# Optimization experiments

Hardware: AMD Instinct MI355X
Metric: run time of the kernel (lower is better)

Reference implementation:

```python
import jax, jax.numpy as jnp
import numpy as np

N_U = 8192
N_C = 8192
D_IN = 32
D_HID = 32  # hidden_dim == output_dim (required by the concat->Linear shape)


def _glorot(key, fan_in, fan_out):
    r = np.sqrt(6.0 / (fan_in + fan_out)).astype(np.float32)
    return jax.random.uniform(key, (fan_in, fan_out), jnp.float32, -r, r)


def setup_inputs() -> dict:
    key = jax.random.key(0)
    ks = jax.random.split(key, 12)
    X_U = jax.random.normal(ks[0], (N_U, D_IN), jnp.float32)
    X_C = jax.random.normal(ks[1], (N_C, D_IN), jnp.float32)
    adj_uu = jax.random.uniform(ks[2], (N_U, N_U), jnp.float32)
    adj_uc = jax.random.uniform(ks[3], (N_U, N_C), jnp.float32)
    adj_cc = jax.random.uniform(ks[4], (N_C, N_C), jnp.float32)
    weight_s = _glorot(ks[5], D_IN, D_HID)          # GCN_S.weight (shared for uu and cc)
    proj_u = _glorot(ks[6], D_IN, D_HID)            # GCN_C.projection_u
    proj_c = _glorot(ks[7], D_IN, D_HID)            # GCN_C.projection_c (unused in fwd math)
    weight_c = _glorot(ks[8], D_HID, D_HID)         # GCN_C.weight
    W_lin = jax.random.normal(ks[9], (D_IN + D_HID, D_HID), jnp.float32) * 0.05  # Linear, no bias
    a_vec = jax.random.normal(ks[10], (D_HID, 1), jnp.float32) * 0.05            # attention vector
    return {"X_U": X_U, "X_C": X_C, "adj_uu": adj_uu, "adj_uc": adj_uc, "adj_cc": adj_cc,
            "weight_s": weight_s, "proj_u": proj_u, "proj_c": proj_c,
            "weight_c": weight_c, "W_lin": W_lin, "a_vec": a_vec}


def gcn_s(adj, x, w):
    # D^-1/2 A D^-1/2 (X W), with D = 1 + rowsum(A); expressed as broadcast scaling
    dinv = jax.lax.rsqrt(1.0 + jnp.sum(adj, axis=1))  # [N]
    support = x @ w                                    # [N, d]
    return dinv[:, None] * (adj @ (dinv[:, None] * support))


def gcn_c(adj, x_u, p_u, w):
    # Du^-1/2 A Dc^-1/2 ((X_U P_u) W); projected_c is computed but unused upstream
    du = jax.lax.rsqrt(jnp.sum(adj, axis=1))  # [N_u]
    dc = jax.lax.rsqrt(jnp.sum(adj, axis=0))  # [N_c]
    support = (x_u @ p_u) @ w                  # [N_u, d]
    return du[:, None] * (adj @ (dc[:, None] * support))  # wait: see note below


def gcn_c_correct(adj, x_u, p_u, w):
    # norm_adj = diag(du) @ adj @ diag(dc)  -> [N_u, N_c]; output = norm_adj @ support ([N_u,d])
    # Actually original multiplies [N_u,N_c] norm_adj by support built from X_U [N_u,d]:
    # this only typechecks when N_u == N_c (as in the repo's usage). We keep that math.
    du = jax.lax.rsqrt(jnp.sum(adj, axis=1))
    dc = jax.lax.rsqrt(jnp.sum(adj, axis=0))
    support = (x_u @ p_u) @ w
    return du[:, None] * (adj @ (dc[:, None] * support))


def reference(X_U, X_C, adj_uu, adj_uc, adj_cc, weight_s, proj_u, proj_c, weight_c, W_lin, a_vec):
    node_embed_u = gcn_s(adj_uu, X_U, weight_s)            # [N_u, d]
    node_embed_c1 = gcn_s(adj_cc, X_C, weight_s)           # [N_c, d]
    node_embed_c2 = gcn_c_correct(adj_uc, X_U, proj_u, weight_c)  # [N_c, d]

    a_tau_1 = jax.nn.relu(jnp.concatenate([node_embed_c1, X_C], axis=-1) @ W_lin) @ a_vec  # [N_c,1]
    a_tau_2 = jax.nn.relu(jnp.concatenate([node_embed_c2, X_C], axis=-1) @ W_lin) @ a_vec  # [N_c,1]
    e_tau = jax.nn.softmax(jnp.concatenate([a_tau_1, a_tau_2], axis=1), axis=1)            # [N_c,2]

    Y_c = e_tau[:, 0:1] * node_embed_c1
    Y_u = e_tau[:, 1:2] * node_embed_c2
    node_embed_c = Y_c + Y_u
    return (node_embed_u, node_embed_c, Y_c, Y_u)
```

## Files before the change

kernel.cpp:

```cpp
#include <hip/hip_runtime.h>
#include <hip/hip_bf16.h>

#define N_NODES 8192

typedef __attribute__((ext_vector_type(8))) short short8;
typedef __attribute__((ext_vector_type(8))) unsigned short ushort8;
typedef __attribute__((ext_vector_type(4))) unsigned short ushort4v;
typedef __attribute__((ext_vector_type(4))) float floatx4;

__device__ inline unsigned short f2bf(float f) {
  unsigned int u = __float_as_uint(f);
  u = (u + 0x7FFFu + ((u >> 16) & 1u)) >> 16;
  return (unsigned short)u;
}

__device__ inline float waveSum(float s) {
#pragma unroll
  for (int off = 32; off >= 1; off >>= 1) s += __shfl_xor(s, off, 64);
  return s;
}

__device__ inline void acc4(float4& a, const float4 b) {
  a.x += b.x; a.y += b.y; a.z += b.z; a.w += b.w;
}
__device__ inline float hsum4(const float4 v) { return v.x + v.y + v.z + v.w; }

__global__ __launch_bounds__(256) void k_rowsum(const float* __restrict__ a_uu,
                                                const float* __restrict__ a_cc,
                                                float* __restrict__ dinv_uu,
                                                float* __restrict__ dinv_cc) {
  const float* A = (blockIdx.y == 0) ? a_uu : a_cc;
  float* dv = (blockIdx.y == 0) ? dinv_uu : dinv_cc;
  int w = threadIdx.x >> 6, l = threadIdx.x & 63;
  long row = (long)blockIdx.x * 4 + w;
  const float* rp = A + row * N_NODES + 4 * l;
  float s = 0.f;
#pragma unroll 2
  for (int i = 0; i < 32; i += 4) {
    float4 v0 = *(const float4*)(rp + 256 * (i + 0));
    float4 v1 = *(const float4*)(rp + 256 * (i + 1));
    float4 v2 = *(const float4*)(rp + 256 * (i + 2));
    float4 v3 = *(const float4*)(rp + 256 * (i + 3));
    s += hsum4(v0) + hsum4(v1) + hsum4(v2) + hsum4(v3);
  }
  s = waveSum(s);
  if (l == 0) dv[row] = rsqrtf(1.0f + s);
}

__global__ __launch_bounds__(256) void k_uc_partials(const float* __restrict__ adj,
                                                     float* __restrict__ rs_part,
                                                     float* __restrict__ cs_part) {
  __shared__ float cacc[4][1024];
  int t = threadIdx.x, w = t >> 6, l = t & 63;
  int rc = blockIdx.x, cc = blockIdx.y;
  int c0 = cc * 1024;
  int rbase = rc * 128 + w * 32;
  float4 ca0 = {0, 0, 0, 0}, ca1 = {0, 0, 0, 0}, ca2 = {0, 0, 0, 0}, ca3 = {0, 0, 0, 0};
  for (int kr = 0; kr < 32; kr += 2) {
    const float* p0 = adj + (long)(rbase + kr) * N_NODES + c0 + 4 * l;
    const float* p1 = p0 + N_NODES;
    float4 u0 = *(const float4*)(p0 + 0);
    float4 u1 = *(const float4*)(p0 + 256);
    float4 u2 = *(const float4*)(p0 + 512);
    float4 u3 = *(const float4*)(p0 + 768);
    float4 v0 = *(const float4*)(p1 + 0);
    float4 v1 = *(const float4*)(p1 + 256);
    float4 v2 = *(const float4*)(p1 + 512);
    float4 v3 = *(const float4*)(p1 + 768);
    acc4(ca0, u0); acc4(ca1, u1); acc4(ca2, u2); acc4(ca3, u3);
    acc4(ca0, v0); acc4(ca1, v1); acc4(ca2, v2); acc4(ca3, v3);
    float s0 = hsum4(u0) + hsum4(u1) + hsum4(u2) + hsum4(u3);
    float s1 = hsum4(v0) + hsum4(v1) + hsum4(v2) + hsum4(v3);
    s0 = waveSum(s0);
    s1 = waveSum(s1);
    if (l == 0) {
      rs_part[(long)cc * N_NODES + rbase + kr] = s0;
      rs_part[(long)cc * N_NODES + rbase + kr + 1] = s1;
    }
  }
  *(float4*)&cacc[w][0 + 4 * l] = ca0;
  *(float4*)&cacc[w][256 + 4 * l] = ca1;
  *(float4*)&cacc[w][512 + 4 * l] = ca2;
  *(float4*)&cacc[w][768 + 4 * l] = ca3;
  __syncthreads();
#pragma unroll
  for (int i = 0; i < 4; ++i) {
    int c = t + 256 * i;
    cs_part[(long)rc * N_NODES + c0 + c] = cacc[0][c] + cacc[1][c] + cacc[2][c] + cacc[3][c];
  }
}

__global__ __launch_bounds__(256) void k_finalize(const float* __restrict__ rs_part,
                                                  const float* __restrict__ cs_part,
                                                  float* __restrict__ du,
                                                  float* __restrict__ dc) {
  int i = blockIdx.x * 256 + threadIdx.x;
  float s = 0.f;
#pragma unroll
  for (int cc = 0; cc < 8; ++cc) s += rs_part[(long)cc * N_NODES + i];
  du[i] = rsqrtf(s);
  float c = 0.f;
#pragma unroll
  for (int rc = 0; rc < 64; ++rc) c += cs_part[(long)rc * N_NODES + i];
  dc[i] = rsqrtf(c);
}

__global__ void k_projw(const float* __restrict__ proj_u,
                        const float* __restrict__ weight_c, float* __restrict__ P) {
  int t = threadIdx.x;
  int i = t >> 5, j = t & 31;
  float s = 0.f;
#pragma unroll
  for (int k = 0; k < 32; ++k) s += proj_u[i * 32 + k] * weight_c[k * 32 + j];
  P[t] = s;
}

__global__ __launch_bounds__(256) void k_support(
    const float* __restrict__ X_U, const float* __restrict__ X_C,
    const float* __restrict__ weight_s, const float* __restrict__ P,
    const float* __restrict__ dinv_uu, const float* __restrict__ dinv_cc,
    const float* __restrict__ dc,
    unsigned short* __restrict__ bt_uu, unsigned short* __restrict__ bt_cc,
    unsigned short* __restrict__ bt_uc) {
  int m = blockIdx.y;
  const float* X = (m == 1) ? X_C : X_U;
  const float* W = (m == 2) ? P : weight_s;
  const float* dv = (m == 0) ? dinv_uu : (m == 1) ? dinv_cc : dc;
  unsigned short* bt = (m == 0) ? bt_uu : (m == 1) ? bt_cc : bt_uc;
  __shared__ float Wl[32][32];
  __shared__ float Xl[8][32];
  int t = threadIdx.x;
#pragma unroll
  for (int i = 0; i < 4; ++i) {
    int idx = t + 256 * i;
    Wl[idx >> 5][idx & 31] = W[idx];
  }
  int r = t >> 5, n = t & 31;
  int j0 = blockIdx.x * 8;
  Xl[r][n] = X[(long)(j0 + r) * 32 + n];
  __syncthreads();
  float s = 0.f;
#pragma unroll
  for (int k = 0; k < 32; ++k) s += Xl[r][k] * Wl[k][n];
  s *= dv[j0 + r];
  bt[(long)n * N_NODES + j0 + r] = f2bf(s);
}

__global__ __launch_bounds__(256) void k_gemm(
    const float* __restrict__ adj_uu, const float* __restrict__ adj_cc,
    const float* __restrict__ adj_uc,
    const unsigned short* __restrict__ bt_uu, const unsigned short* __restrict__ bt_cc,
    const unsigned short* __restrict__ bt_uc,
    const float* __restrict__ dinv_uu, const float* __restrict__ dinv_cc,
    const float* __restrict__ du,
    float* __restrict__ out_u, float* __restrict__ c1, float* __restrict__ c2) {
  int m = blockIdx.y;
  const float* adj = (m == 0) ? adj_uu : (m == 1) ? adj_cc : adj_uc;
  const unsigned short* bt = (m == 0) ? bt_uu : (m == 1) ? bt_cc : bt_uc;
  const float* dsc = (m == 0) ? dinv_uu : (m == 1) ? dinv_cc : du;
  float* outp = (m == 0) ? out_u : (m == 1) ? c1 : c2;

  __shared__ unsigned short As[32][136];
  __shared__ unsigned short Bs[32][136];

  int t = threadIdx.x;
  int w = t >> 6, l = t & 63;
  int mh = w & 1, nh = w >> 1;
  long r0 = (long)blockIdx.x * 32;

  int ar = t >> 3, ac = (t & 7) * 4;
  int bn = t >> 3, bk = (t & 7) * 8;

  const float* ap = adj + (r0 + ar) * N_NODES + ac;
  const unsigned short* bp = bt + (long)bn * N_NODES + bk;

  float4 a0 = *(const float4*)(ap + 0);
  float4 a1 = *(const float4*)(ap + 32);
  float4 a2 = *(const float4*)(ap + 64);
  float4 a3 = *(const float4*)(ap + 96);
  ushort8 b0 = *(const ushort8*)(bp + 0);
  ushort8 b1 = *(const ushort8*)(bp + 64);

  floatx4 acc = {0.f, 0.f, 0.f, 0.f};

  for (int step = 0; step < 64; ++step) {
    ushort4v q;
    q.x = f2bf(a0.x); q.y = f2bf(a0.y); q.z = f2bf(a0.z); q.w = f2bf(a0.w);
    *(ushort4v*)&As[ar][ac + 0] = q;
    q.x = f2bf(a1.x); q.y = f2bf(a1.y); q.z = f2bf(a1.z); q.w = f2bf(a1.w);
    *(ushort4v*)&As[ar][ac + 32] = q;
    q.x = f2bf(a2.x); q.y = f2bf(a2.y); q.z = f2bf(a2.z); q.w = f2bf(a2.w);
    *(ushort4v*)&As[ar][ac + 64] = q;
    q.x = f2bf(a3.x); q.y = f2bf(a3.y); q.z = f2bf(a3.z); q.w = f2bf(a3.w);
    *(ushort4v*)&As[ar][ac + 96] = q;
    *(ushort8*)&Bs[bn][bk + 0] = b0;
    *(ushort8*)&Bs[bn][bk + 64] = b1;
    __syncthreads();

    if (step < 63) {
      ap += 128; bp += 128;
      a0 = *(const float4*)(ap + 0);
      a1 = *(const float4*)(ap + 32);
      a2 = *(const float4*)(ap + 64);
      a3 = *(const float4*)(ap + 96);
      b0 = *(const ushort8*)(bp + 0);
      b1 = *(const ushort8*)(bp + 64);
    }

#pragma unroll
    for (int kk = 0; kk < 4; ++kk) {
      short8 af = *(const short8*)&As[16 * mh + (l & 15)][kk * 32 + (l >> 4) * 8];
      short8 bf = *(const short8*)&Bs[16 * nh + (l & 15)][kk * 32 + (l >> 4) * 8];
      acc = __builtin_amdgcn_mfma_f32_16x16x32_bf16(af, bf, acc, 0, 0, 0);
    }
    __syncthreads();
  }

  int mrow = (int)r0 + 16 * mh + ((l >> 4) << 2);
  int ncol = 16 * nh + (l & 15);
#pragma unroll
  for (int r = 0; r < 4; ++r) {
    float sc = dsc[mrow + r];
    outp[(long)(mrow + r) * 32 + ncol] = sc * acc[r];
  }
}

__global__ __launch_bounds__(256) void k_epilogue(
    const float* __restrict__ c1, const float* __restrict__ c2,
    const float* __restrict__ X_C, const float* __restrict__ W_lin,
    const float* __restrict__ a_vec, float* __restrict__ out) {
  __shared__ float Wl[64][32];
  __shared__ float al[32];
  int t = threadIdx.x;
#pragma unroll
  for (int i = 0; i < 8; ++i) {
    int idx = t + 256 * i;
    Wl[idx >> 5][idx & 31] = W_lin[idx];
  }
  if (t < 32) al[t] = a_vec[t];
  int g = t >> 5, n = t & 31;
  long row = (long)blockIdx.x * 8 + g;
  __syncthreads();
  float h1 = c1[row * 32 + n];
  float h2 = c2[row * 32 + n];
  float xv = X_C[row * 32 + n];
  float s1 = 0.f, s2 = 0.f, sx = 0.f;
#pragma unroll
  for (int k = 0; k < 32; ++k) {
    float h1k = __shfl(h1, k, 32);
    float h2k = __shfl(h2, k, 32);
    float xk = __shfl(xv, k, 32);
    float w0 = Wl[k][n], w1 = Wl[32 + k][n];
    s1 += h1k * w0;
    s2 += h2k * w0;
    sx += xk * w1;
  }
  float t1 = fmaxf(s1 + sx, 0.f) * al[n];
  float t2 = fmaxf(s2 + sx, 0.f) * al[n];
#pragma unroll
  for (int off = 16; off >= 1; off >>= 1) {
    t1 += __shfl_xor(t1, off, 32);
    t2 += __shfl_xor(t2, off, 32);
  }
  float mx = fmaxf(t1, t2);
  float e1 = expf(t1 - mx), e2 = expf(t2 - mx);
  float inv = 1.0f / (e1 + e2);
  float w1w = e1 * inv, w2w = e2 * inv;
  float yc = w1w * h1, yu = w2w * h2;
  long o = row * 32 + n;
  out[262144 + o] = yc + yu;
  out[524288 + o] = yc;
  out[786432 + o] = yu;
}

extern "C" void kernel_launch(void* const* d_in, const int* in_sizes, int n_in,
                              void* d_out, int out_size, void* d_ws, size_t ws_size,
                              hipStream_t stream) {
  (void)in_sizes; (void)n_in; (void)out_size; (void)ws_size;
  const float* X_U = (const float*)d_in[0];
  const float* X_C = (const float*)d_in[1];
  const float* adj_uu = (const float*)d_in[2];
  const float* adj_uc = (const float*)d_in[3];
  const float* adj_cc = (const float*)d_in[4];
  const float* weight_s = (const float*)d_in[5];
  const float* proj_u = (const float*)d_in[6];
  const float* weight_c = (const float*)d_in[8];
  const float* W_lin = (const float*)d_in[9];
  const float* a_vec = (const float*)d_in[10];
  float* out = (float*)d_out;

  char* ws = (char*)d_ws;
  auto alloc = [&](size_t bytes) {
    char* p = ws;
    ws += (bytes + 255) & ~(size_t)255;
    return p;
  };
  float* dinv_uu = (float*)alloc(8192 * 4);
  float* dinv_cc = (float*)alloc(8192 * 4);
  float* du = (float*)alloc(8192 * 4);
  float* dc = (float*)alloc(8192 * 4);
  float* rs_part = (float*)alloc((size_t)8 * 8192 * 4);
  float* cs_part = (float*)alloc((size_t)64 * 8192 * 4);
  float* P = (float*)alloc(1024 * 4);
  float* c1 = (float*)alloc((size_t)262144 * 4);
  float* c2 = (float*)alloc((size_t)262144 * 4);
  unsigned short* bt_uu = (unsigned short*)alloc((size_t)262144 * 2);
  unsigned short* bt_cc = (unsigned short*)alloc((size_t)262144 * 2);
  unsigned short* bt_uc = (unsigned short*)alloc((size_t)262144 * 2);

  hipLaunchKernelGGL(k_rowsum, dim3(2048, 2), dim3(256), 0, stream,
                     adj_uu, adj_cc, dinv_uu, dinv_cc);
  hipLaunchKernelGGL(k_uc_partials, dim3(64, 8), dim3(256), 0, stream,
                     adj_uc, rs_part, cs_part);
  hipLaunchKernelGGL(k_finalize, dim3(32), dim3(256), 0, stream,
                     rs_part, cs_part, du, dc);
  hipLaunchKernelGGL(k_projw, dim3(1), dim3(1024), 0, stream, proj_u, weight_c, P);
  hipLaunchKernelGGL(k_support, dim3(1024, 3), dim3(256), 0, stream,
                     X_U, X_C, weight_s, P, dinv_uu, dinv_cc, dc, bt_uu, bt_cc, bt_uc);
  hipLaunchKernelGGL(k_gemm, dim3(256, 3), dim3(256), 0, stream,
                     adj_uu, adj_cc, adj_uc, bt_uu, bt_cc, bt_uc,
                     dinv_uu, dinv_cc, du, out, c1, c2);
  hipLaunchKernelGGL(k_epilogue, dim3(1024), dim3(256), 0, stream,
                     c1, c2, X_C, W_lin, a_vec, out);
}
```

Measured before the change: 847.5 us.

## Replace LDS-tiled GEMM with single-wave register MFMA kernel and split-K partials

After: 877.8 us. 3.6% more time.

```diff
diff --git a/kernel.cpp b/kernel.cpp
--- a/kernel.cpp
+++ b/kernel.cpp
@@ -4,8 +4,6 @@
 #define N_NODES 8192
 
 typedef __attribute__((ext_vector_type(8))) short short8;
-typedef __attribute__((ext_vector_type(8))) unsigned short ushort8;
-typedef __attribute__((ext_vector_type(4))) unsigned short ushort4v;
 typedef __attribute__((ext_vector_type(4))) float floatx4;
 
 __device__ inline unsigned short f2bf(float f) {
@@ -14,6 +12,15 @@
   return (unsigned short)u;
 }
 
+__device__ inline short8 cvt8(const float4 lo, const float4 hi) {
+  short8 r;
+  r[0] = (short)f2bf(lo.x); r[1] = (short)f2bf(lo.y);
+  r[2] = (short)f2bf(lo.z); r[3] = (short)f2bf(lo.w);
+  r[4] = (short)f2bf(hi.x); r[5] = (short)f2bf(hi.y);
+  r[6] = (short)f2bf(hi.z); r[7] = (short)f2bf(hi.w);
+  return r;
+}
+
 __device__ inline float waveSum(float s) {
 #pragma unroll
   for (int off = 32; off >= 1; off >>= 1) s += __shfl_xor(s, off, 64);
@@ -25,12 +32,8 @@
 }
 __device__ inline float hsum4(const float4 v) { return v.x + v.y + v.z + v.w; }
 
-__global__ __launch_bounds__(256) void k_rowsum(const float* __restrict__ a_uu,
-                                                const float* __restrict__ a_cc,
-                                                float* __restrict__ dinv_uu,
-                                                float* __restrict__ dinv_cc) {
-  const float* A = (blockIdx.y == 0) ? a_uu : a_cc;
-  float* dv = (blockIdx.y == 0) ? dinv_uu : dinv_cc;
+__global__ __launch_bounds__(256) void k_rowsum(const float* __restrict__ A,
+                                                float* __restrict__ dv) {
   int w = threadIdx.x >> 6, l = threadIdx.x & 63;
   long row = (long)blockIdx.x * 4 + w;
   const float* rp = A + row * N_NODES + 4 * l;
@@ -115,18 +118,10 @@
   P[t] = s;
 }
 
-__global__ __launch_bounds__(256) void k_support(
-    const float* __restrict__ X_U, const float* __restrict__ X_C,
-    const float* __restrict__ weight_s, const float* __restrict__ P,
-    const float* __restrict__ dinv_uu, const float* __restrict__ dinv_cc,
-    const float* __restrict__ dc,
-    unsigned short* __restrict__ bt_uu, unsigned short* __restrict__ bt_cc,
-    unsigned short* __restrict__ bt_uc) {
-  int m = blockIdx.y;
-  const float* X = (m == 1) ? X_C : X_U;
-  const float* W = (m == 2) ? P : weight_s;
-  const float* dv = (m == 0) ? dinv_uu : (m == 1) ? dinv_cc : dc;
-  unsigned short* bt = (m == 0) ? bt_uu : (m == 1) ? bt_cc : bt_uc;
+__global__ __launch_bounds__(256) void k_support(const float* __restrict__ X,
+                                                 const float* __restrict__ W,
+                                                 const float* __restrict__ dv,
+                                                 short* __restrict__ bt) {
   __shared__ float Wl[32][32];
   __shared__ float Xl[8][32];
   int t = threadIdx.x;
@@ -143,90 +138,71 @@
 #pragma unroll
   for (int k = 0; k < 32; ++k) s += Xl[r][k] * Wl[k][n];
   s *= dv[j0 + r];
-  bt[(long)n * N_NODES + j0 + r] = f2bf(s);
-}
-
-__global__ __launch_bounds__(256) void k_gemm(
-    const float* __restrict__ adj_uu, const float* __restrict__ adj_cc,
-    const float* __restrict__ adj_uc,
-    const unsigned short* __restrict__ bt_uu, const unsigned short* __restrict__ bt_cc,
-    const unsigned short* __restrict__ bt_uc,
-    const float* __restrict__ dinv_uu, const float* __restrict__ dinv_cc,
-    const float* __restrict__ du,
-    float* __restrict__ out_u, float* __restrict__ c1, float* __restrict__ c2) {
-  int m = blockIdx.y;
-  const float* adj = (m == 0) ? adj_uu : (m == 1) ? adj_cc : adj_uc;
-  const unsigned short* bt = (m == 0) ? bt_uu : (m == 1) ? bt_cc : bt_uc;
-  const float* dsc = (m == 0) ? dinv_uu : (m == 1) ? dinv_cc : du;
-  float* outp = (m == 0) ? out_u : (m == 1) ? c1 : c2;
-
-  __shared__ unsigned short As[32][136];
-  __shared__ unsigned short Bs[32][136];
-
-  int t = threadIdx.x;
-  int w = t >> 6, l = t & 63;
-  int mh = w & 1, nh = w >> 1;
-  long r0 = (long)blockIdx.x * 32;
-
-  int ar = t >> 3, ac = (t & 7) * 4;
-  int bn = t >> 3, bk = (t & 7) * 8;
-
-  const float* ap = adj + (r0 + ar) * N_NODES + ac;
-  const unsigned short* bp = bt + (long)bn * N_NODES + bk;
-
-  float4 a0 = *(const float4*)(ap + 0);
-  float4 a1 = *(const float4*)(ap + 32);
-  float4 a2 = *(const float4*)(ap + 64);
-  float4 a3 = *(const float4*)(ap + 96);
-  ushort8 b0 = *(const ushort8*)(bp + 0);
-  ushort8 b1 = *(const ushort8*)(bp + 64);
-
-  floatx4 acc = {0.f, 0.f, 0.f, 0.f};
-
-  for (int step = 0; step < 64; ++step) {
-    ushort4v q;
-    q.x = f2bf(a0.x); q.y = f2bf(a0.y); q.z = f2bf(a0.z); q.w = f2bf(a0.w);
-    *(ushort4v*)&As[ar][ac + 0] = q;
-    q.x = f2bf(a1.x); q.y = f2bf(a1.y); q.z = f2bf(a1.z); q.w = f2bf(a1.w);
-    *(ushort4v*)&As[ar][ac + 32] = q;
-    q.x = f2bf(a2.x); q.y = f2bf(a2.y); q.z = f2bf(a2.z); q.w = f2bf(a2.w);
-    *(ushort4v*)&As[ar][ac + 64] = q;
-    q.x = f2bf(a3.x); q.y = f2bf(a3.y); q.z = f2bf(a3.z); q.w = f2bf(a3.w);
-    *(ushort4v*)&As[ar][ac + 96] = q;
-    *(ushort8*)&Bs[bn][bk + 0] = b0;
-    *(ushort8*)&Bs[bn][bk + 64] = b1;
-    __syncthreads();
-
-    if (step < 63) {
-      ap += 128; bp += 128;
-      a0 = *(const float4*)(ap + 0);
-      a1 = *(const float4*)(ap + 32);
-      a2 = *(const float4*)(ap + 64);
-      a3 = *(const float4*)(ap + 96);
-      b0 = *(const ushort8*)(bp + 0);
-      b1 = *(const ushort8*)(bp + 64);
-    }
-
-#pragma unroll
-    for (int kk = 0; kk < 4; ++kk) {
-      short8 af = *(const short8*)&As[16 * mh + (l & 15)][kk * 32 + (l >> 4) * 8];
-      short8 bf = *(const short8*)&Bs[16 * nh + (l & 15)][kk * 32 + (l >> 4) * 8];
-      acc = __builtin_amdgcn_mfma_f32_16x16x32_bf16(af, bf, acc, 0, 0, 0);
-    }
-    __syncthreads();
-  }
-
-  int mrow = (int)r0 + 16 * mh + ((l >> 4) << 2);
-  int ncol = 16 * nh + (l & 15);
+  bt[(long)n * N_NODES + j0 + r] = (short)f2bf(s);
+}
+
+__global__ __launch_bounds__(64) void k_gemm_wave(const float* __restrict__ adj,
+                                                  const short* __restrict__ bt,
+                                                  float* __restrict__ part) {
+  int l = threadIdx.x;
+  int bx = blockIdx.x;
+  int kh = bx & 1;
+  long r0 = (long)(bx >> 1) * 16;
+  int m = l & 15, q = l >> 4;
+
+  const float* ap = adj + (r0 + m) * N_NODES + kh * 4096 + q * 8;
+  const short* b0p = bt + (long)m * N_NODES + kh * 4096 + q * 8;
+  const short* b1p = b0p + 16L * N_NODES;
+
+  floatx4 acc0 = {0.f, 0.f, 0.f, 0.f}, acc1 = {0.f, 0.f, 0.f, 0.f};
+
+  float4 c0lo = *(const float4*)(ap + 0);
+  float4 c0hi = *(const float4*)(ap + 4);
+  short8 d00 = *(const short8*)(b0p + 0);
+  short8 d10 = *(const short8*)(b1p + 0);
+  float4 c1lo = *(const float4*)(ap + 32);
+  float4 c1hi = *(const float4*)(ap + 36);
+  short8 d01 = *(const short8*)(b0p + 32);
+  short8 d11 = *(const short8*)(b1p + 32);
+
+  for (int it = 0; it < 63; ++it) {
+    ap += 64; b0p += 64; b1p += 64;
+    short8 af0 = cvt8(c0lo, c0hi);
+    acc0 = __builtin_amdgcn_mfma_f32_16x16x32_bf16(af0, d00, acc0, 0, 0, 0);
+    acc1 = __builtin_amdgcn_mfma_f32_16x16x32_bf16(af0, d10, acc1, 0, 0, 0);
+    c0lo = *(const float4*)(ap + 0);
+    c0hi = *(const float4*)(ap + 4);
+    d00 = *(const short8*)(b0p + 0);
+    d10 = *(const short8*)(b1p + 0);
+    short8 af1 = cvt8(c1lo, c1hi);
+    acc0 = __builtin_amdgcn_mfma_f32_16x16x32_bf16(af1, d01, acc0, 0, 0, 0);
+    acc1 = __builtin_amdgcn_mfma_f32_16x16x32_bf16(af1, d11, acc1, 0, 0, 0);
+    c1lo = *(const float4*)(ap + 32);
+    c1hi = *(const float4*)(ap + 36);
+    d01 = *(const short8*)(b0p + 32);
+    d11 = *(const short8*)(b1p + 32);
+  }
+  {
+    short8 af0 = cvt8(c0lo, c0hi);
+    acc0 = __builtin_amdgcn_mfma_f32_16x16x32_bf16(af0, d00, acc0, 0, 0, 0);
+    acc1 = __builtin_amdgcn_mfma_f32_16x16x32_bf16(af0, d10, acc1, 0, 0, 0);
+    short8 af1 = cvt8(c1lo, c1hi);
+    acc0 = __builtin_amdgcn_mfma_f32_16x16x32_bf16(af1, d01, acc0, 0, 0, 0);
+    acc1 = __builtin_amdgcn_mfma_f32_16x16x32_bf16(af1, d11, acc1, 0, 0, 0);
+  }
+
+  float* pp = part + (long)kh * 262144 + (r0 + q * 4) * 32;
 #pragma unroll
   for (int r = 0; r < 4; ++r) {
-    float sc = dsc[mrow + r];
-    outp[(long)(mrow + r) * 32 + ncol] = sc * acc[r];
+    pp[r * 32 + m] = acc0[r];
+    pp[r * 32 + 16 + m] = acc1[r];
   }
 }
 
 __global__ __launch_bounds__(256) void k_epilogue(
-    const float* __restrict__ c1, const float* __restrict__ c2,
+    const float* __restrict__ pu, const float* __restrict__ pc,
+    const float* __restrict__ pq, const float* __restrict__ dinv_uu,
+    const float* __restrict__ dinv_cc, const float* __restrict__ du,
     const float* __restrict__ X_C, const float* __restrict__ W_lin,
     const float* __restrict__ a_vec, float* __restrict__ out) {
   __shared__ float Wl[64][32];
@@ -240,10 +216,14 @@
   if (t < 32) al[t] = a_vec[t];
   int g = t >> 5, n = t & 31;
   long row = (long)blockIdx.x * 8 + g;
+  long o = row * 32 + n;
   __syncthreads();
-  float h1 = c1[row * 32 + n];
-  float h2 = c2[row * 32 + n];
-  float xv = X_C[row * 32 + n];
+
+  out[o] = dinv_uu[row] * (pu[o] + pu[262144 + o]);
+
+  float h1 = dinv_cc[row] * (pc[o] + pc[262144 + o]);
+  float h2 = du[row] * (pq[o] + pq[262144 + o]);
+  float xv = X_C[o];
   float s1 = 0.f, s2 = 0.f, sx = 0.f;
 #pragma unroll
   for (int k = 0; k < 32; ++k) {
@@ -265,9 +245,7 @@
   float mx = fmaxf(t1, t2);
   float e1 = expf(t1 - mx), e2 = expf(t2 - mx);
   float inv = 1.0f / (e1 + e2);
-  float w1w = e1 * inv, w2w = e2 * inv;
-  float yc = w1w * h1, yu = w2w * h2;
-  long o = row * 32 + n;
+  float yc = e1 * inv * h1, yu = e2 * inv * h2;
   out[262144 + o] = yc + yu;
   out[524288 + o] = yc;
   out[786432 + o] = yu;
@@ -302,24 +280,32 @@
   float* rs_part = (float*)alloc((size_t)8 * 8192 * 4);
   float* cs_part = (float*)alloc((size_t)64 * 8192 * 4);
   float* P = (float*)alloc(1024 * 4);
-  float* c1 = (float*)alloc((size_t)262144 * 4);
-  float* c2 = (float*)alloc((size_t)262144 * 4);
-  unsigned short* bt_uu = (unsigned short*)alloc((size_t)262144 * 2);
-  unsigned short* bt_cc = (unsigned short*)alloc((size_t)262144 * 2);
-  unsigned short* bt_uc = (unsigned short*)alloc((size_t)262144 * 2);
-
-  hipLaunchKernelGGL(k_rowsum, dim3(2048, 2), dim3(256), 0, stream,
-                     adj_uu, adj_cc, dinv_uu, dinv_cc);
+  float* pu = (float*)alloc((size_t)2 * 262144 * 4);
+  float* pc = (float*)alloc((size_t)2 * 262144 * 4);
+  float* pq = (float*)alloc((size_t)2 * 262144 * 4);
+  short* bt_uu = (short*)alloc((size_t)262144 * 2);
+  short* bt_cc = (short*)alloc((size_t)262144 * 2);
+  short* bt_uc = (short*)alloc((size_t)262144 * 2);
+
+  hipLaunchKernelGGL(k_projw, dim3(1), dim3(1024), 0, stream, proj_u, weight_c, P);
+
+  hipLaunchKernelGGL(k_rowsum, dim3(2048), dim3(256), 0, stream, adj_uu, dinv_uu);
+  hipLaunchKernelGGL(k_support, dim3(1024), dim3(256), 0, stream,
+                     X_U, weight_s, dinv_uu, bt_uu);
+  hipLaunchKernelGGL(k_gemm_wave, dim3(1024), dim3(64), 0, stream, adj_uu, bt_uu, pu);
+
+  hipLaunchKernelGGL(k_rowsum, dim3(2048), dim3(256), 0, stream, adj_cc, dinv_cc);
+  hipLaunchKernelGGL(k_support, dim3(1024), dim3(256), 0, stream,
+                     X_C, weight_s, dinv_cc, bt_cc);
+  hipLaunchKernelGGL(k_gemm_wave, dim3(1024), dim3(64), 0, stream, adj_cc, bt_cc, pc);
+
   hipLaunchKernelGGL(k_uc_partials, dim3(64, 8), dim3(256), 0, stream,
                      adj_uc, rs_part, cs_part);
   hipLaunchKernelGGL(k_finalize, dim3(32), dim3(256), 0, stream,
                      rs_part, cs_part, du, dc);
-  hipLaunchKernelGGL(k_projw, dim3(1), dim3(1024), 0, stream, proj_u, weight_c, P);
-  hipLaunchKernelGGL(k_support, dim3(1024, 3), dim3(256), 0, stream,
-                     X_U, X_C, weight_s, P, dinv_uu, dinv_cc, dc, bt_uu, bt_cc, bt_uc);
-  hipLaunchKernelGGL(k_gemm, dim3(256, 3), dim3(256), 0, stream,
-                     adj_uu, adj_cc, adj_uc, bt_uu, bt_cc, bt_uc,
-                     dinv_uu, dinv_cc, du, out, c1, c2);
+  hipLaunchKernelGGL(k_support, dim3(1024), dim3(256), 0, stream, X_U, P, dc, bt_uc);
+  hipLaunchKernelGGL(k_gemm_wave, dim3(1024), dim3(64), 0, stream, adj_uc, bt_uc, pq);
+
   hipLaunchKernelGGL(k_epilogue, dim3(1024), dim3(256), 0, stream,
-                     c1, c2, X_C, W_lin, a_vec, out);
-}
+                     pu, pc, pq, dinv_uu, dinv_cc, du, X_C, W_lin, a_vec, out);
+}
```
